# Optimization experiments

Measured on AMD Instinct MI355X. Metric: run time of the kernel, lower is better.

The kernel has to match this reference:

```python
import jax, jax.numpy as jnp
import numpy as np

HAD_BLOCK = 1024  # had_block_size


def _fwht(x):
    """Fast Walsh-Hadamard transform over last dim (power of 2), unnormalized."""
    m, n = x.shape
    h = 1
    while h < n:  # log2(n) static iterations
        x = x.reshape(m, n // (2 * h), 2, h)
        a = x[:, :, 0, :]
        b = x[:, :, 1, :]
        x = jnp.stack([a + b, a - b], axis=2)
        h *= 2
    return x.reshape(m, n)


def blockwise_hadamard(x, block):
    shape = x.shape
    xb = x.reshape(-1, block)
    xb = _fwht(xb) * (1.0 / np.sqrt(block)).astype(np.float32)
    return xb.reshape(shape)


def setup_inputs() -> dict:
    key = jax.random.key(0)
    k1, k2, k3 = jax.random.split(key, 3)
    B, S, D_IN, D_OUT = 2, 4096, 4096, 4096
    x = jax.random.normal(k1, (B, S, D_IN), dtype=jnp.float32)
    W = jax.random.normal(k2, (D_OUT, D_IN), dtype=jnp.float32) * 0.02
    b = jax.random.normal(k3, (D_OUT,), dtype=jnp.float32) * 0.02
    return {"x": x, "W": W, "b": b}


def reference(x, W, b):
    # blockwise FHT on input, then dense linear y = xh @ W^T + b
    xh = blockwise_hadamard(x, HAD_BLOCK)
    return jnp.einsum('bsd,od->bso', xh, W) + b
```

## Files before the change

kernel.cpp:

```cpp
#include <hip/hip_runtime.h>
#include <hip/hip_bf16.h>

typedef short s16x8 __attribute__((ext_vector_type(8)));
typedef float f32x4 __attribute__((ext_vector_type(4)));

__device__ __forceinline__ unsigned short f2bf(float f) {
  unsigned u = __float_as_uint(f);
  u += 0x7fffu + ((u >> 16) & 1u);
  return (unsigned short)(u >> 16);
}

__device__ __forceinline__ void gload16(const void* g, void* l) {
  __builtin_amdgcn_global_load_lds(
      (const __attribute__((address_space(1))) unsigned int*)g,
      (__attribute__((address_space(3))) unsigned int*)l,
      16, 0, 0);
}

__global__ void __launch_bounds__(256) k_pre(const float* __restrict__ W,
                                             unsigned short* __restrict__ Wh,
                                             const float* __restrict__ x,
                                             unsigned short* __restrict__ xb,
                                             int nblk_w, long n4) {
  __shared__ float s[1024];
  const int t = threadIdx.x;

  if (blockIdx.x < nblk_w) {
    const size_t base = (size_t)blockIdx.x * 1024;

    float4 v = reinterpret_cast<const float4*>(W + base)[t];
    s[4 * t + 0] = v.x;
    s[4 * t + 1] = v.y;
    s[4 * t + 2] = v.z;
    s[4 * t + 3] = v.w;

#pragma unroll
    for (int h = 1; h < 1024; h <<= 1) {
      __syncthreads();
#pragma unroll
      for (int pp = 0; pp < 2; ++pp) {
        int p = t + pp * 256;
        int i = ((p / h) * (h << 1)) + (p % h);
        float a = s[i], b = s[i + h];
        s[i] = a + b;
        s[i + h] = a - b;
      }
    }
    __syncthreads();

    const float sc = 0.03125f;
    ushort4 o;
    o.x = f2bf(s[4 * t + 0] * sc);
    o.y = f2bf(s[4 * t + 1] * sc);
    o.z = f2bf(s[4 * t + 2] * sc);
    o.w = f2bf(s[4 * t + 3] * sc);
    reinterpret_cast<ushort4*>(Wh + base)[t] = o;
  } else {
    long i = (long)(blockIdx.x - nblk_w) * 256 + t;
    const long stride = (long)(gridDim.x - nblk_w) * 256;
    for (; i < n4; i += stride) {
      float4 v = reinterpret_cast<const float4*>(x)[i];
      ushort4 o;
      o.x = f2bf(v.x);
      o.y = f2bf(v.y);
      o.z = f2bf(v.z);
      o.w = f2bf(v.w);
      reinterpret_cast<ushort4*>(xb)[i] = o;
    }
  }
}


#define STAGE_HALF(gbase, halfRow, koff, ldsDst)                             \
  do {                                                                       \
    gload16(gbase + (size_t)(halfRow)*K + (koff), (ldsDst) + tid * 16);      \
    gload16(gbase + (size_t)((halfRow) + 64)*K + (koff),                     \
            (ldsDst) + 8192 + tid * 16);                                     \
  } while (0)

#define RD_AF0(bufp)                                                         \
  do { _Pragma("unroll")                                                     \
    for (int i = 0; i < 4; ++i) {                                            \
      af0[i][0] = *(const s16x8*)((bufp) + aoff0 + i * 2048);                \
      af0[i][1] = *(const s16x8*)((bufp) + aoff1 + i * 2048);                \
    } } while (0)

#define RD_AF1(bufp)                                                         \
  do { _Pragma("unroll")                                                     \
    for (int i = 0; i < 4; ++i) {                                            \
      af1[i][0] = *(const s16x8*)((bufp) + aoff0 + 8192 + i * 2048);         \
      af1[i][1] = *(const s16x8*)((bufp) + aoff1 + 8192 + i * 2048);         \
    } } while (0)

#define RD_BF0(bufp)                                                         \
  do { _Pragma("unroll")                                                     \
    for (int j2 = 0; j2 < 2; ++j2) {                                         \
      bf0[j2][0] = *(const s16x8*)((bufp) + boff0 + j2 * 2048);              \
      bf0[j2][1] = *(const s16x8*)((bufp) + boff1 + j2 * 2048);              \
    } } while (0)

#define RD_BF1(bufp)                                                         \
  do { _Pragma("unroll")                                                     \
    for (int j2 = 0; j2 < 2; ++j2) {                                         \
      bf1[j2][0] = *(const s16x8*)((bufp) + boff0 + 4096 + j2 * 2048);       \
      bf1[j2][1] = *(const s16x8*)((bufp) + boff1 + 4096 + j2 * 2048);       \
    } } while (0)

#define MFMA_Q(msel, nsel, AF, BF)                                           \
  do {                                                                       \
    __builtin_amdgcn_s_setprio(1);                                           \
    _Pragma("unroll")                                                        \
    for (int kk = 0; kk < 2; ++kk) {                                         \
      _Pragma("unroll")                                                      \
      for (int i = 0; i < 4; ++i) {                                          \
        _Pragma("unroll")                                                    \
        for (int j2 = 0; j2 < 2; ++j2) {                                     \
          acc[(msel)*4 + i][(nsel)*2 + j2] =                                 \
            __builtin_amdgcn_mfma_f32_16x16x32_bf16(                         \
              AF[i][kk], BF[j2][kk], acc[(msel)*4 + i][(nsel)*2 + j2],       \
              0, 0, 0);                                                      \
        }                                                                    \
      }                                                                      \
    }                                                                        \
    __builtin_amdgcn_s_setprio(0);                                           \
  } while (0)

#define BAR() __builtin_amdgcn_s_barrier()

__global__ void __launch_bounds__(512, 2) k_gemm256(
    const unsigned short* __restrict__ A, const unsigned short* __restrict__ B,
    const float* __restrict__ bias, float* __restrict__ C,
    int M, int N, int K) {
  __shared__ char LDS[163840];

  const int tid = threadIdx.x;
  const int lane = tid & 63;
  const int wid = tid >> 6;
  const int wm = wid >> 2;
  const int wn = wid & 3;
  const int fr = lane & 15;
  const int fq = lane >> 4;

  const int nbn = N >> 8;
  const int cpx = gridDim.x >> 3;
  const int swz = (blockIdx.x & 7) * cpx + (blockIdx.x >> 3);
  const int bm = swz / nbn, bn = swz % nbn;

  const int r0 = tid >> 3;
  const int ck = (tid & 7) ^ (r0 & 7);
  const unsigned short* gAbase = A + (size_t)(bm * 256 + r0) * K + ck * 8;
  const unsigned short* gBbase = B + (size_t)(bn * 256 + r0) * K + ck * 8;

  const int cs0 = ((fq ^ (fr & 7)) << 4);
  const int cs1 = (((fq + 4) ^ (fr & 7)) << 4);
  const int aoff0 = wm * 16384 + fr * 128 + cs0;
  const int aoff1 = wm * 16384 + fr * 128 + cs1;
  const int bbase0 = (wn >> 1) * 16384 + (wn & 1) * 8192 + fr * 128;
  const int boff0 = bbase0 + cs0;
  const int boff1 = bbase0 + cs1;

  f32x4 acc[8][4];
#pragma unroll
  for (int m = 0; m < 8; ++m)
#pragma unroll
    for (int n = 0; n < 4; ++n)
      acc[m][n] = (f32x4){0.f, 0.f, 0.f, 0.f};

  s16x8 af0[4][2], af1[4][2], bf0[2][2], bf1[2][2];

  STAGE_HALF(gAbase, 0,   0, LDS);
  STAGE_HALF(gAbase, 128, 0, LDS + 16384);
  STAGE_HALF(gBbase, 0,   0, LDS + 98304);
  STAGE_HALF(gBbase, 128, 0, LDS + 98304 + 16384);
  STAGE_HALF(gAbase, 0,   64, LDS + 32768);
  STAGE_HALF(gAbase, 128, 64, LDS + 32768 + 16384);
  STAGE_HALF(gBbase, 0,   64, LDS + 131072);
  STAGE_HALF(gBbase, 128, 64, LDS + 131072 + 16384);
  asm volatile("s_waitcnt vmcnt(8)" ::: "memory");
  BAR();
  RD_AF0(LDS);
  RD_BF0(LDS + 98304);

  const int nt = K >> 6;
  int am = 0, an = 1, an2 = 2;
  for (int t = 0; t < nt; ++t) {
    const char* bA  = LDS + am * 32768;
    const char* bAn = LDS + an * 32768;
    char*       bAs = LDS + an2 * 32768;
    const char* bB  = LDS + 98304 + ((t & 1) << 15);
    const char* bBn = LDS + 98304 + (((t + 1) & 1) << 15);
    char*       bBs = (char*)bB;
    const int koff2 = (t + 2) << 6;

    RD_BF1(bB);
    RD_AF1(bA);
    if (t + 2 < nt) STAGE_HALF(gAbase, 0, koff2, bAs);
    BAR();
    MFMA_Q(0, 0, af0, bf0);

    if (t + 2 < nt) STAGE_HALF(gAbase, 128, koff2, bAs + 16384);
    BAR();
    MFMA_Q(0, 1, af0, bf1);

    if (t + 2 < nt) STAGE_HALF(gBbase, 0, koff2, bBs);
    BAR();
    MFMA_Q(1, 0, af1, bf0);

    if (t + 2 < nt) STAGE_HALF(gBbase, 128, koff2, bBs + 16384);
    if (t < nt - 2) {
      asm volatile("s_waitcnt vmcnt(8)" ::: "memory");
    } else if (t == nt - 2) {
      asm volatile("s_waitcnt vmcnt(0)" ::: "memory");
    }
    BAR();
    if (t + 1 < nt) {
      RD_AF0(bAn);
      RD_BF0(bBn);
    }
    MFMA_Q(1, 1, af1, bf1);

    const int tmp = am;
    am = an; an = an2; an2 = tmp;
  }

  const int row0 = bm * 256 + wm * 128;
  const int col0 = bn * 256 + wn * 64;
  float bv[4];
#pragma unroll
  for (int nf = 0; nf < 4; ++nf) bv[nf] = bias[col0 + nf * 16 + fr];

#pragma unroll
  for (int mf = 0; mf < 8; ++mf) {
#pragma unroll
    for (int nf = 0; nf < 4; ++nf) {
#pragma unroll
      for (int i = 0; i < 4; ++i) {
        const int r = row0 + mf * 16 + fq * 4 + i;
        const int c = col0 + nf * 16 + fr;
        C[(size_t)r * N + c] = acc[mf][nf][i] + bv[nf];
      }
    }
  }
}

extern "C" void kernel_launch(void* const* d_in, const int* in_sizes, int n_in,
                              void* d_out, int out_size, void* d_ws, size_t ws_size,
                              hipStream_t stream) {
  const float* x = (const float*)d_in[0];
  const float* W = (const float*)d_in[1];
  const float* b = (const float*)d_in[2];
  float* out = (float*)d_out;

  const int N = in_sizes[2];
  const int K = in_sizes[1] / N;
  const int M = in_sizes[0] / K;

  unsigned short* Xb = (unsigned short*)d_ws;
  unsigned short* Wh = Xb + (size_t)M * K;

  const int nblk_w = (int)(((size_t)N * K) / 1024);
  const long n4 = ((long)M * K) / 4;
  k_pre<<<nblk_w + 4096, 256, 0, stream>>>(W, Wh, x, Xb, nblk_w, n4);

  const int grid = (M / 256) * (N / 256);
  k_gemm256<<<grid, 512, 0, stream>>>(Xb, Wh, b, out, M, N, K);
}
```

Before: 279.3 us.

## Restructure GEMM main loop to double-buffered 8-phase schedule with smaller LDS

Replaces the triple-buffered A / double-buffered B pipeline with a two-buffer ping-pong for both operands. The loop is unrolled by two K-tiles and split into eight barrier-separated phases that interleave LDS fragment reads, global-to-LDS staging and MFMA quarters, with explicit lgkmcnt/vmcnt waits. This cuts LDS from 160KB to 128KB and mirrors a known HipKittens-style 8-wave schedule. It adds many more barriers and less prefetch depth, which risks exposing load latency.

```diff
diff --git a/kernel.cpp b/kernel.cpp
--- a/kernel.cpp
+++ b/kernel.cpp
@@ -126,12 +126,13 @@
   } while (0)
 
 #define BAR() __builtin_amdgcn_s_barrier()
+#define LGKM0() asm volatile("s_waitcnt lgkmcnt(0)" ::: "memory")
 
 __global__ void __launch_bounds__(512, 2) k_gemm256(
     const unsigned short* __restrict__ A, const unsigned short* __restrict__ B,
     const float* __restrict__ bias, float* __restrict__ C,
     int M, int N, int K) {
-  __shared__ char LDS[163840];
+  __shared__ char LDS[131072];
 
   const int tid = threadIdx.x;
   const int lane = tid & 63;
@@ -159,6 +160,11 @@
   const int boff0 = bbase0 + cs0;
   const int boff1 = bbase0 + cs1;
 
+  char* const bA0 = LDS;
+  char* const bA1 = LDS + 32768;
+  char* const bB0 = LDS + 65536;
+  char* const bB1 = LDS + 98304;
+
   f32x4 acc[8][4];
 #pragma unroll
   for (int m = 0; m < 8; ++m)
@@ -168,59 +174,92 @@
 
   s16x8 af0[4][2], af1[4][2], bf0[2][2], bf1[2][2];
 
-  STAGE_HALF(gAbase, 0,   0, LDS);
-  STAGE_HALF(gAbase, 128, 0, LDS + 16384);
-  STAGE_HALF(gBbase, 0,   0, LDS + 98304);
-  STAGE_HALF(gBbase, 128, 0, LDS + 98304 + 16384);
-  STAGE_HALF(gAbase, 0,   64, LDS + 32768);
-  STAGE_HALF(gAbase, 128, 64, LDS + 32768 + 16384);
-  STAGE_HALF(gBbase, 0,   64, LDS + 131072);
-  STAGE_HALF(gBbase, 128, 64, LDS + 131072 + 16384);
-  asm volatile("s_waitcnt vmcnt(8)" ::: "memory");
+  STAGE_HALF(gAbase, 0,   0,  bA0);
+  STAGE_HALF(gAbase, 128, 0,  bA0 + 16384);
+  STAGE_HALF(gBbase, 0,   0,  bB0);
+  STAGE_HALF(gBbase, 128, 0,  bB0 + 16384);
+  STAGE_HALF(gBbase, 0,   64, bB1);
+  STAGE_HALF(gBbase, 128, 64, bB1 + 16384);
+  STAGE_HALF(gAbase, 0,   64, bA1);
+  asm volatile("s_waitcnt vmcnt(6)" ::: "memory");
   BAR();
-  RD_AF0(LDS);
-  RD_BF0(LDS + 98304);
 
   const int nt = K >> 6;
-  int am = 0, an = 1, an2 = 2;
-  for (int t = 0; t < nt; ++t) {
-    const char* bA  = LDS + am * 32768;
-    const char* bAn = LDS + an * 32768;
-    char*       bAs = LDS + an2 * 32768;
-    const char* bB  = LDS + 98304 + ((t & 1) << 15);
-    const char* bBn = LDS + 98304 + (((t + 1) & 1) << 15);
-    char*       bBs = (char*)bB;
-    const int koff2 = (t + 2) << 6;
-
-    RD_BF1(bB);
-    RD_AF1(bA);
-    if (t + 2 < nt) STAGE_HALF(gAbase, 0, koff2, bAs);
-    BAR();
+  const int ni = nt >> 1;
+  for (int i = 0; i < ni; ++i) {
+    const int t1k = (2 * i + 1) << 6;
+    const int t2k = (2 * i + 2) << 6;
+    const int t3k = (2 * i + 3) << 6;
+    const bool s23 = (2 * i + 2) < nt;
+    const bool last = (i == ni - 1);
+
+    RD_AF0(bA0);
+    RD_BF0(bB0);
+    STAGE_HALF(gAbase, 128, t1k, bA1 + 16384);
+    asm volatile("s_waitcnt lgkmcnt(8)" ::: "memory");
+    BAR();
+    LGKM0();
     MFMA_Q(0, 0, af0, bf0);
-
-    if (t + 2 < nt) STAGE_HALF(gAbase, 128, koff2, bAs + 16384);
-    BAR();
+    BAR();
+
+    RD_BF1(bB0);
+    BAR();
+    LGKM0();
     MFMA_Q(0, 1, af0, bf1);
-
-    if (t + 2 < nt) STAGE_HALF(gBbase, 0, koff2, bBs);
-    BAR();
+    BAR();
+
+    RD_AF1(bA0);
+    if (s23) {
+      STAGE_HALF(gBbase, 0,   t2k, bB0);
+      STAGE_HALF(gBbase, 128, t2k, bB0 + 16384);
+    }
+    BAR();
+    LGKM0();
     MFMA_Q(1, 0, af1, bf0);
-
-    if (t + 2 < nt) STAGE_HALF(gBbase, 128, koff2, bBs + 16384);
-    if (t < nt - 2) {
-      asm volatile("s_waitcnt vmcnt(8)" ::: "memory");
-    } else if (t == nt - 2) {
+    BAR();
+
+    if (s23) STAGE_HALF(gAbase, 0, t2k, bA0);
+    if (!last) {
+      asm volatile("s_waitcnt vmcnt(6)" ::: "memory");
+    } else {
       asm volatile("s_waitcnt vmcnt(0)" ::: "memory");
     }
     BAR();
-    if (t + 1 < nt) {
-      RD_AF0(bAn);
-      RD_BF0(bBn);
-    }
     MFMA_Q(1, 1, af1, bf1);
-
-    const int tmp = am;
-    am = an; an = an2; an2 = tmp;
+    BAR();
+
+    RD_AF0(bA1);
+    RD_BF0(bB1);
+    if (s23) STAGE_HALF(gAbase, 128, t2k, bA0 + 16384);
+    asm volatile("s_waitcnt lgkmcnt(8)" ::: "memory");
+    BAR();
+    LGKM0();
+    MFMA_Q(0, 0, af0, bf0);
+    BAR();
+
+    RD_BF1(bB1);
+    BAR();
+    LGKM0();
+    MFMA_Q(0, 1, af0, bf1);
+    BAR();
+
+    RD_AF1(bA1);
+    if (s23) {
+      STAGE_HALF(gBbase, 0,   t3k, bB1);
+      STAGE_HALF(gBbase, 128, t3k, bB1 + 16384);
+    }
+    BAR();
+    LGKM0();
+    MFMA_Q(1, 0, af1, bf0);
+    BAR();
+
+    if (s23) STAGE_HALF(gAbase, 0, t3k, bA1);
+    if (!last) {
+      asm volatile("s_waitcnt vmcnt(6)" ::: "memory");
+    }
+    BAR();
+    MFMA_Q(1, 1, af1, bf1);
+    BAR();
   }
 
   const int row0 = bm * 256 + wm * 128;
```

New measurement: 290.4 us. 4.0% more time.
